# Performance work log

Hardware: AMD Instinct MI355X
Metric: run time of the kernel (lower is better)

## Reference

```python
import jax, jax.numpy as jnp
import numpy as np

BLOCK = 100  # hard-coded block size in the original module


def setup_inputs() -> dict:
    key = jax.random.key(0)
    k1, k2 = jax.random.split(key)
    N_freqs = 128
    n = N_freqs * BLOCK  # 12800
    # DPP kernel: symmetric PD so every 100x100 diagonal block has positive logdet
    R = jax.random.normal(k1, (n, n), dtype=jnp.float32) * 0.05
    L_kernel = (R + R.T) * 0.5 + 2.0 * jnp.eye(n, dtype=jnp.float32)
    weights = jax.random.normal(k2, (n,), dtype=jnp.float32)
    return {"weights": weights, "L_kernel": L_kernel, "N_freqs": N_freqs}


def reference(weights, L_kernel, N_freqs):
    # Gather the N_freqs diagonal 100x100 blocks without touching off-diagonals
    blocks4 = L_kernel.reshape(N_freqs, BLOCK, N_freqs, BLOCK)
    idx = jnp.arange(N_freqs)
    diag_blocks = blocks4[idx, :, idx, :]  # [N_freqs, 100, 100]
    s = jax.nn.sigmoid(weights).reshape(N_freqs, BLOCK)  # [N_freqs, 100]
    I = jnp.eye(BLOCK, dtype=L_kernel.dtype)
    # diag(s_i) @ (B_i - I) + I, batched over blocks
    M = s[:, :, None] * (diag_blocks - I) + I  # [N_freqs, 100, 100]
    sign, logabs = jnp.linalg.slogdet(M)
    # torch.logdet returns nan for non-positive determinant
    logdets = jnp.where(sign > 0, logabs, jnp.nan)
    within_freq_dets = jnp.sum(logdets)
    within_freq_dets_tensor = logdets.astype(jnp.float32)
    return (within_freq_dets, within_freq_dets_tensor)
```

## Files before the change

### kernel.cpp

```cpp
#include <hip/hip_runtime.h>
#include <math.h>

#define BLK 100
#define NF  128
#define NTOT (NF * BLK)
#define P   104
#define NT  512

__device__ __forceinline__ float4 fnma4(float4 v, float s, const float4 p) {
    v.x -= s * p.x; v.y -= s * p.y; v.z -= s * p.z; v.w -= s * p.w; return v;
}
__device__ __forceinline__ float4 mul4(float4 v, float s) {
    v.x *= s; v.y *= s; v.z *= s; v.w *= s; return v;
}

#define LD4(r, c4) (*reinterpret_cast<float4*>(&a[(r) * P + 4 * (c4)]))

#define PANEL_Q(kb, gq)                                                        \
    {                                                                          \
        float4 pp0 = LD4((kb) + 0, (gq));                                      \
        float4 pp1 = LD4((kb) + 1, (gq));                                      \
        float4 pp2 = LD4((kb) + 2, (gq));                                      \
        float4 pp3 = LD4((kb) + 3, (gq));                                      \
        float4 P0  = LD4((kb) + 0, gg);                                        \
        float4 P1  = LD4((kb) + 1, gg);                                        \
        float4 P2  = LD4((kb) + 2, gg);                                        \
        float4 P3  = LD4((kb) + 3, gg);                                        \
        const float d0 = pp0.x, r0i = 1.0f / d0;                               \
        float l;                                                               \
        l = pp1.x * r0i;  pp1 = fnma4(pp1, l, pp0);  P1 = fnma4(P1, l, P0);    \
        const float d1 = pp1.y, r1i = 1.0f / d1;                               \
        l = pp2.x * r0i;  pp2 = fnma4(pp2, l, pp0);  P2 = fnma4(P2, l, P0);    \
        l = pp2.y * r1i;  pp2 = fnma4(pp2, l, pp1);  P2 = fnma4(P2, l, P1);    \
        const float d2 = pp2.z, r2i = 1.0f / d2;                               \
        l = pp3.x * r0i;  pp3 = fnma4(pp3, l, pp0);  P3 = fnma4(P3, l, P0);    \
        l = pp3.y * r1i;  pp3 = fnma4(pp3, l, pp1);  P3 = fnma4(P3, l, P1);    \
        l = pp3.z * r2i;  pp3 = fnma4(pp3, l, pp2);  P3 = fnma4(P3, l, P2);    \
        const float d3 = pp3.w, r3i = 1.0f / d3;                               \
        Q3 = mul4(P3, r3i);                                                    \
        Q2 = mul4(fnma4(P2, pp2.w, Q3), r2i);                                  \
        Q1 = mul4(fnma4(fnma4(P1, pp1.z, Q2), pp1.w, Q3), r1i);                \
        Q0 = mul4(fnma4(fnma4(fnma4(P0, pp0.y, Q1), pp0.z, Q2), pp0.w, Q3), r0i); \
        mant *= d0 * d1 * d2 * d3;                                             \
        { int t_; mant = frexpf(mant, &t_); e2 += t_; }                        \
        lneg += (d0 < 0.0f) + (d1 < 0.0f) + (d2 < 0.0f) + (d3 < 0.0f);         \
    }

__global__ __launch_bounds__(NT) void lu_logdet_kernel(const float* __restrict__ w,
                                                       const float* __restrict__ L,
                                                       float* __restrict__ out) {
    __shared__ float  a[BLK * P];
    __shared__ float4 qbuf[2][4][26];

    const int f    = blockIdx.x;
    const int tid  = threadIdx.x;
    const int wave = tid >> 6;
    const int sid  = tid >> 5;
    const int g    = tid & 31;
    const int gg   = (g < 25) ? g : 24;

    const float* base = L + (size_t)f * BLK * NTOT + (size_t)f * BLK;
    for (int q = tid; q < BLK * 25; q += NT) {
        const int r  = q / 25;
        const int c0 = (q - r * 25) * 4;
        const float4 v = *reinterpret_cast<const float4*>(base + (size_t)r * NTOT + c0);
        const float sv = 1.0f / (1.0f + expf(-w[f * BLK + r]));
        const float ds = 1.0f - sv;
        float4 m;
        m.x = sv * v.x + ((c0 + 0) == r ? ds : 0.0f);
        m.y = sv * v.y + ((c0 + 1) == r ? ds : 0.0f);
        m.z = sv * v.z + ((c0 + 2) == r ? ds : 0.0f);
        m.w = sv * v.w + ((c0 + 3) == r ? ds : 0.0f);
        *reinterpret_cast<float4*>(&a[r * P + c0]) = m;
    }
    __syncthreads();

    float mant = 1.0f;
    int   e2   = 0;
    int   lneg = 0;
    float4 Q0, Q1, Q2, Q3;

    PANEL_Q(0, 0)

    for (int k0 = 0; k0 <= 92; k0 += 4) {
        const int gp = k0 >> 2;
        const int b  = gp & 1;
        const int nb = b ^ 1;

        if (wave == 0) {
            __builtin_amdgcn_s_setprio(1);
            if (g > gp && g < 25) {
                const int s  = sid & 1;
                const int i1 = k0 + 4 + s;
                const int i2 = k0 + 6 + s;
                const float4 pan1 = LD4(i1, gp);
                const float4 pan2 = LD4(i2, gp);
                float4 v1 = LD4(i1, g);
                float4 v2 = LD4(i2, g);
                v1 = fnma4(v1, pan1.x, Q0); v1 = fnma4(v1, pan1.y, Q1);
                v1 = fnma4(v1, pan1.z, Q2); v1 = fnma4(v1, pan1.w, Q3);
                v2 = fnma4(v2, pan2.x, Q0); v2 = fnma4(v2, pan2.y, Q1);
                v2 = fnma4(v2, pan2.z, Q2); v2 = fnma4(v2, pan2.w, Q3);
                LD4(i1, g) = v1;
                LD4(i2, g) = v2;
            }
            PANEL_Q(k0 + 4, gp + 1)
            if (g < 25) {
                qbuf[nb][0][g] = Q0; qbuf[nb][1][g] = Q1;
                qbuf[nb][2][g] = Q2; qbuf[nb][3][g] = Q3;
            }
            __builtin_amdgcn_s_setprio(0);
        } else {
            if (k0 > 0) {
                Q0 = qbuf[b][0][gg]; Q1 = qbuf[b][1][gg];
                Q2 = qbuf[b][2][gg]; Q3 = qbuf[b][3][gg];
            }
            if (g > gp && g < 25) {
                int i = k0 + 8 + (sid - 2);
                for (; i + 14 < BLK; i += 28) {
                    const int i2 = i + 14;
                    const float4 panA = LD4(i,  gp);
                    const float4 panB = LD4(i2, gp);
                    float4 vA = LD4(i,  g);
                    float4 vB = LD4(i2, g);
                    vA = fnma4(vA, panA.x, Q0); vA = fnma4(vA, panA.y, Q1);
                    vA = fnma4(vA, panA.z, Q2); vA = fnma4(vA, panA.w, Q3);
                    vB = fnma4(vB, panB.x, Q0); vB = fnma4(vB, panB.y, Q1);
                    vB = fnma4(vB, panB.z, Q2); vB = fnma4(vB, panB.w, Q3);
                    LD4(i,  g) = vA;
                    LD4(i2, g) = vB;
                }
                for (; i < BLK; i += 14) {
                    const float4 pan = LD4(i, gp);
                    float4 v = LD4(i, g);
                    v = fnma4(v, pan.x, Q0); v = fnma4(v, pan.y, Q1);
                    v = fnma4(v, pan.z, Q2); v = fnma4(v, pan.w, Q3);
                    LD4(i, g) = v;
                }
            }
        }
        __syncthreads();
    }

    if (tid == 0) {
        float ld = logf(mant) + (float)e2 * 0.69314718055994531f;
        if ((lneg & 1) || !isfinite(ld)) ld = __int_as_float(0x7fc00000);
        out[1 + f] = ld;
        atomicAdd(out, ld);
    }
}

extern "C" void kernel_launch(void* const* d_in, const int* in_sizes, int n_in,
                              void* d_out, int out_size, void* d_ws, size_t ws_size,
                              hipStream_t stream) {
    const float* w = (const float*)d_in[0];
    const float* L = (const float*)d_in[1];
    float* out = (float*)d_out;
    hipMemsetAsync(d_out, 0, sizeof(float), stream);
    lu_logdet_kernel<<<NF, NT, 0, stream>>>(w, L, out);
}
```

Measured before the change: 30.43 us.

## Widen blocked LU panel from 4 to 8 columns to halve barrier steps

```diff
diff --git a/kernel.cpp b/kernel.cpp
--- a/kernel.cpp
+++ b/kernel.cpp
@@ -16,41 +16,75 @@
 
 #define LD4(r, c4) (*reinterpret_cast<float4*>(&a[(r) * P + 4 * (c4)]))
 
-#define PANEL_Q(kb, gq)                                                        \
-    {                                                                          \
-        float4 pp0 = LD4((kb) + 0, (gq));                                      \
-        float4 pp1 = LD4((kb) + 1, (gq));                                      \
-        float4 pp2 = LD4((kb) + 2, (gq));                                      \
-        float4 pp3 = LD4((kb) + 3, (gq));                                      \
-        float4 P0  = LD4((kb) + 0, gg);                                        \
-        float4 P1  = LD4((kb) + 1, gg);                                        \
-        float4 P2  = LD4((kb) + 2, gg);                                        \
-        float4 P3  = LD4((kb) + 3, gg);                                        \
-        const float d0 = pp0.x, r0i = 1.0f / d0;                               \
-        float l;                                                               \
-        l = pp1.x * r0i;  pp1 = fnma4(pp1, l, pp0);  P1 = fnma4(P1, l, P0);    \
-        const float d1 = pp1.y, r1i = 1.0f / d1;                               \
-        l = pp2.x * r0i;  pp2 = fnma4(pp2, l, pp0);  P2 = fnma4(P2, l, P0);    \
-        l = pp2.y * r1i;  pp2 = fnma4(pp2, l, pp1);  P2 = fnma4(P2, l, P1);    \
-        const float d2 = pp2.z, r2i = 1.0f / d2;                               \
-        l = pp3.x * r0i;  pp3 = fnma4(pp3, l, pp0);  P3 = fnma4(P3, l, P0);    \
-        l = pp3.y * r1i;  pp3 = fnma4(pp3, l, pp1);  P3 = fnma4(P3, l, P1);    \
-        l = pp3.z * r2i;  pp3 = fnma4(pp3, l, pp2);  P3 = fnma4(P3, l, P2);    \
-        const float d3 = pp3.w, r3i = 1.0f / d3;                               \
-        Q3 = mul4(P3, r3i);                                                    \
-        Q2 = mul4(fnma4(P2, pp2.w, Q3), r2i);                                  \
-        Q1 = mul4(fnma4(fnma4(P1, pp1.z, Q2), pp1.w, Q3), r1i);                \
-        Q0 = mul4(fnma4(fnma4(fnma4(P0, pp0.y, Q1), pp0.z, Q2), pp0.w, Q3), r0i); \
-        mant *= d0 * d1 * d2 * d3;                                             \
-        { int t_; mant = frexpf(mant, &t_); e2 += t_; }                        \
-        lneg += (d0 < 0.0f) + (d1 < 0.0f) + (d2 < 0.0f) + (d3 < 0.0f);         \
-    }
-
-__global__ __launch_bounds__(NT) void lu_logdet_kernel(const float* __restrict__ w,
-                                                       const float* __restrict__ L,
-                                                       float* __restrict__ out) {
+#define PANEL_Q8(kb, q2)                                                        \
+    {                                                                           \
+        float4 pA0 = LD4((kb)+0, (q2)), pB0 = LD4((kb)+0, (q2)+1);              \
+        float4 pA1 = LD4((kb)+1, (q2)), pB1 = LD4((kb)+1, (q2)+1);              \
+        float4 pA2 = LD4((kb)+2, (q2)), pB2 = LD4((kb)+2, (q2)+1);              \
+        float4 pA3 = LD4((kb)+3, (q2)), pB3 = LD4((kb)+3, (q2)+1);              \
+        float4 pA4 = LD4((kb)+4, (q2)), pB4 = LD4((kb)+4, (q2)+1);              \
+        float4 pA5 = LD4((kb)+5, (q2)), pB5 = LD4((kb)+5, (q2)+1);              \
+        float4 pA6 = LD4((kb)+6, (q2)), pB6 = LD4((kb)+6, (q2)+1);              \
+        float4 pA7 = LD4((kb)+7, (q2)), pB7 = LD4((kb)+7, (q2)+1);              \
+        float4 P0 = LD4((kb)+0, gg), P1 = LD4((kb)+1, gg);                      \
+        float4 P2 = LD4((kb)+2, gg), P3 = LD4((kb)+3, gg);                      \
+        float4 P4 = LD4((kb)+4, gg), P5 = LD4((kb)+5, gg);                      \
+        float4 P6 = LD4((kb)+6, gg), P7 = LD4((kb)+7, gg);                      \
+        const float d0 = pA0.x, r0 = 1.0f / d0;                                 \
+        float l;                                                                \
+        l = pA1.x*r0; pA1=fnma4(pA1,l,pA0); pB1=fnma4(pB1,l,pB0); P1=fnma4(P1,l,P0); \
+        l = pA2.x*r0; pA2=fnma4(pA2,l,pA0); pB2=fnma4(pB2,l,pB0); P2=fnma4(P2,l,P0); \
+        l = pA3.x*r0; pA3=fnma4(pA3,l,pA0); pB3=fnma4(pB3,l,pB0); P3=fnma4(P3,l,P0); \
+        l = pA4.x*r0; pA4=fnma4(pA4,l,pA0); pB4=fnma4(pB4,l,pB0); P4=fnma4(P4,l,P0); \
+        l = pA5.x*r0; pA5=fnma4(pA5,l,pA0); pB5=fnma4(pB5,l,pB0); P5=fnma4(P5,l,P0); \
+        l = pA6.x*r0; pA6=fnma4(pA6,l,pA0); pB6=fnma4(pB6,l,pB0); P6=fnma4(P6,l,P0); \
+        l = pA7.x*r0; pA7=fnma4(pA7,l,pA0); pB7=fnma4(pB7,l,pB0); P7=fnma4(P7,l,P0); \
+        const float d1 = pA1.y, r1 = 1.0f / d1;                                 \
+        l = pA2.y*r1; pA2=fnma4(pA2,l,pA1); pB2=fnma4(pB2,l,pB1); P2=fnma4(P2,l,P1); \
+        l = pA3.y*r1; pA3=fnma4(pA3,l,pA1); pB3=fnma4(pB3,l,pB1); P3=fnma4(P3,l,P1); \
+        l = pA4.y*r1; pA4=fnma4(pA4,l,pA1); pB4=fnma4(pB4,l,pB1); P4=fnma4(P4,l,P1); \
+        l = pA5.y*r1; pA5=fnma4(pA5,l,pA1); pB5=fnma4(pB5,l,pB1); P5=fnma4(P5,l,P1); \
+        l = pA6.y*r1; pA6=fnma4(pA6,l,pA1); pB6=fnma4(pB6,l,pB1); P6=fnma4(P6,l,P1); \
+        l = pA7.y*r1; pA7=fnma4(pA7,l,pA1); pB7=fnma4(pB7,l,pB1); P7=fnma4(P7,l,P1); \
+        const float d2 = pA2.z, r2 = 1.0f / d2;                                 \
+        l = pA3.z*r2; pA3=fnma4(pA3,l,pA2); pB3=fnma4(pB3,l,pB2); P3=fnma4(P3,l,P2); \
+        l = pA4.z*r2; pA4=fnma4(pA4,l,pA2); pB4=fnma4(pB4,l,pB2); P4=fnma4(P4,l,P2); \
+        l = pA5.z*r2; pA5=fnma4(pA5,l,pA2); pB5=fnma4(pB5,l,pB2); P5=fnma4(P5,l,P2); \
+        l = pA6.z*r2; pA6=fnma4(pA6,l,pA2); pB6=fnma4(pB6,l,pB2); P6=fnma4(P6,l,P2); \
+        l = pA7.z*r2; pA7=fnma4(pA7,l,pA2); pB7=fnma4(pB7,l,pB2); P7=fnma4(P7,l,P2); \
+        const float d3 = pA3.w, r3 = 1.0f / d3;                                 \
+        l = pA4.w*r3; pB4=fnma4(pB4,l,pB3); P4=fnma4(P4,l,P3);                  \
+        l = pA5.w*r3; pB5=fnma4(pB5,l,pB3); P5=fnma4(P5,l,P3);                  \
+        l = pA6.w*r3; pB6=fnma4(pB6,l,pB3); P6=fnma4(P6,l,P3);                  \
+        l = pA7.w*r3; pB7=fnma4(pB7,l,pB3); P7=fnma4(P7,l,P3);                  \
+        const float d4 = pB4.x, r4 = 1.0f / d4;                                 \
+        l = pB5.x*r4; pB5=fnma4(pB5,l,pB4); P5=fnma4(P5,l,P4);                  \
+        l = pB6.x*r4; pB6=fnma4(pB6,l,pB4); P6=fnma4(P6,l,P4);                  \
+        l = pB7.x*r4; pB7=fnma4(pB7,l,pB4); P7=fnma4(P7,l,P4);                  \
+        const float d5 = pB5.y, r5 = 1.0f / d5;                                 \
+        l = pB6.y*r5; pB6=fnma4(pB6,l,pB5); P6=fnma4(P6,l,P5);                  \
+        l = pB7.y*r5; pB7=fnma4(pB7,l,pB5); P7=fnma4(P7,l,P5);                  \
+        const float d6 = pB6.z, r6 = 1.0f / d6;                                 \
+        l = pB7.z*r6; pB7=fnma4(pB7,l,pB6); P7=fnma4(P7,l,P6);                  \
+        const float d7 = pB7.w, r7 = 1.0f / d7;                                 \
+        Q7 = mul4(P7, r7);                                                      \
+        Q6 = mul4(fnma4(P6, pB6.w, Q7), r6);                                    \
+        Q5 = mul4(fnma4(fnma4(P5, pB5.z, Q6), pB5.w, Q7), r5);                  \
+        Q4 = mul4(fnma4(fnma4(fnma4(P4, pB4.y, Q5), pB4.z, Q6), pB4.w, Q7), r4); \
+        Q3 = mul4(fnma4(fnma4(fnma4(fnma4(P3, pB3.x, Q4), pB3.y, Q5), pB3.z, Q6), pB3.w, Q7), r3); \
+        Q2 = mul4(fnma4(fnma4(fnma4(fnma4(fnma4(P2, pA2.w, Q3), pB2.x, Q4), pB2.y, Q5), pB2.z, Q6), pB2.w, Q7), r2); \
+        Q1 = mul4(fnma4(fnma4(fnma4(fnma4(fnma4(fnma4(P1, pA1.z, Q2), pA1.w, Q3), pB1.x, Q4), pB1.y, Q5), pB1.z, Q6), pB1.w, Q7), r1); \
+        Q0 = mul4(fnma4(fnma4(fnma4(fnma4(fnma4(fnma4(fnma4(P0, pA0.y, Q1), pA0.z, Q2), pA0.w, Q3), pB0.x, Q4), pB0.y, Q5), pB0.z, Q6), pB0.w, Q7), r0); \
+        mant *= d0 * d1 * d2 * d3; { int t_; mant = frexpf(mant, &t_); e2 += t_; } \
+        mant *= d4 * d5 * d6 * d7; { int t_; mant = frexpf(mant, &t_); e2 += t_; } \
+        lneg += (d0<0.0f)+(d1<0.0f)+(d2<0.0f)+(d3<0.0f)+(d4<0.0f)+(d5<0.0f)+(d6<0.0f)+(d7<0.0f); \
+    }
+
+__global__ __launch_bounds__(NT, 2) void lu_logdet_kernel(const float* __restrict__ w,
+                                                          const float* __restrict__ L,
+                                                          float* __restrict__ out) {
     __shared__ float  a[BLK * P];
-    __shared__ float4 qbuf[2][4][26];
+    __shared__ float4 qbuf[2][8][26];
 
     const int f    = blockIdx.x;
     const int tid  = threadIdx.x;
@@ -78,63 +112,96 @@
     float mant = 1.0f;
     int   e2   = 0;
     int   lneg = 0;
-    float4 Q0, Q1, Q2, Q3;
-
-    PANEL_Q(0, 0)
-
-    for (int k0 = 0; k0 <= 92; k0 += 4) {
-        const int gp = k0 >> 2;
-        const int b  = gp & 1;
+    float4 Q0, Q1, Q2, Q3, Q4, Q5, Q6, Q7;
+
+    PANEL_Q8(0, 0)
+
+    for (int k0 = 0; k0 <= 88; k0 += 8) {
+        const int pc = k0 >> 2;
+        const int b  = (k0 >> 3) & 1;
         const int nb = b ^ 1;
 
         if (wave == 0) {
             __builtin_amdgcn_s_setprio(1);
-            if (g > gp && g < 25) {
-                const int s  = sid & 1;
-                const int i1 = k0 + 4 + s;
-                const int i2 = k0 + 6 + s;
-                const float4 pan1 = LD4(i1, gp);
-                const float4 pan2 = LD4(i2, gp);
-                float4 v1 = LD4(i1, g);
-                float4 v2 = LD4(i2, g);
-                v1 = fnma4(v1, pan1.x, Q0); v1 = fnma4(v1, pan1.y, Q1);
-                v1 = fnma4(v1, pan1.z, Q2); v1 = fnma4(v1, pan1.w, Q3);
-                v2 = fnma4(v2, pan2.x, Q0); v2 = fnma4(v2, pan2.y, Q1);
-                v2 = fnma4(v2, pan2.z, Q2); v2 = fnma4(v2, pan2.w, Q3);
-                LD4(i1, g) = v1;
-                LD4(i2, g) = v2;
-            }
-            PANEL_Q(k0 + 4, gp + 1)
             if (g < 25) {
-                qbuf[nb][0][g] = Q0; qbuf[nb][1][g] = Q1;
-                qbuf[nb][2][g] = Q2; qbuf[nb][3][g] = Q3;
+                const int rbase = k0 + 8 + ((sid & 1) << 2);
+                #pragma unroll
+                for (int j = 0; j < 4; ++j) {
+                    const int r = rbase + j;
+                    if (r < BLK) {
+                        const float4 pA = LD4(r, pc);
+                        const float4 pB = LD4(r, pc + 1);
+                        float4 v = LD4(r, g);
+                        v = fnma4(v, pA.x, Q0); v = fnma4(v, pA.y, Q1);
+                        v = fnma4(v, pA.z, Q2); v = fnma4(v, pA.w, Q3);
+                        v = fnma4(v, pB.x, Q4); v = fnma4(v, pB.y, Q5);
+                        v = fnma4(v, pB.z, Q6); v = fnma4(v, pB.w, Q7);
+                        LD4(r, g) = v;
+                    }
+                }
+            }
+            if (k0 < 88) {
+                PANEL_Q8(k0 + 8, pc + 2)
+                if (g < 25) {
+                    qbuf[nb][0][g] = Q0; qbuf[nb][1][g] = Q1;
+                    qbuf[nb][2][g] = Q2; qbuf[nb][3][g] = Q3;
+                    qbuf[nb][4][g] = Q4; qbuf[nb][5][g] = Q5;
+                    qbuf[nb][6][g] = Q6; qbuf[nb][7][g] = Q7;
+                }
+            } else {
+                float4 t0 = LD4(96, 24), t1 = LD4(97, 24), t2 = LD4(98, 24), t3 = LD4(99, 24);
+                const float d0 = t0.x, r0 = 1.0f / d0;
+                float l;
+                l = t1.x*r0; t1 = fnma4(t1, l, t0);
+                l = t2.x*r0; t2 = fnma4(t2, l, t0);
+                l = t3.x*r0; t3 = fnma4(t3, l, t0);
+                const float d1 = t1.y, r1 = 1.0f / d1;
+                l = t2.y*r1; t2 = fnma4(t2, l, t1);
+                l = t3.y*r1; t3 = fnma4(t3, l, t1);
+                const float d2 = t2.z, r2 = 1.0f / d2;
+                l = t3.z*r2; t3 = fnma4(t3, l, t2);
+                const float d3 = t3.w;
+                mant *= d0 * d1 * d2 * d3;
+                { int t_; mant = frexpf(mant, &t_); e2 += t_; }
+                lneg += (d0<0.0f)+(d1<0.0f)+(d2<0.0f)+(d3<0.0f);
             }
             __builtin_amdgcn_s_setprio(0);
         } else {
             if (k0 > 0) {
                 Q0 = qbuf[b][0][gg]; Q1 = qbuf[b][1][gg];
                 Q2 = qbuf[b][2][gg]; Q3 = qbuf[b][3][gg];
-            }
-            if (g > gp && g < 25) {
-                int i = k0 + 8 + (sid - 2);
+                Q4 = qbuf[b][4][gg]; Q5 = qbuf[b][5][gg];
+                Q6 = qbuf[b][6][gg]; Q7 = qbuf[b][7][gg];
+            }
+            if (g < 25) {
+                int i = k0 + 16 + (sid - 2);
                 for (; i + 14 < BLK; i += 28) {
                     const int i2 = i + 14;
-                    const float4 panA = LD4(i,  gp);
-                    const float4 panB = LD4(i2, gp);
+                    const float4 pA1_ = LD4(i,  pc);
+                    const float4 pB1_ = LD4(i,  pc + 1);
+                    const float4 pA2_ = LD4(i2, pc);
+                    const float4 pB2_ = LD4(i2, pc + 1);
                     float4 vA = LD4(i,  g);
                     float4 vB = LD4(i2, g);
-                    vA = fnma4(vA, panA.x, Q0); vA = fnma4(vA, panA.y, Q1);
-                    vA = fnma4(vA, panA.z, Q2); vA = fnma4(vA, panA.w, Q3);
-                    vB = fnma4(vB, panB.x, Q0); vB = fnma4(vB, panB.y, Q1);
-                    vB = fnma4(vB, panB.z, Q2); vB = fnma4(vB, panB.w, Q3);
+                    vA = fnma4(vA, pA1_.x, Q0); vA = fnma4(vA, pA1_.y, Q1);
+                    vA = fnma4(vA, pA1_.z, Q2); vA = fnma4(vA, pA1_.w, Q3);
+                    vA = fnma4(vA, pB1_.x, Q4); vA = fnma4(vA, pB1_.y, Q5);
+                    vA = fnma4(vA, pB1_.z, Q6); vA = fnma4(vA, pB1_.w, Q7);
+                    vB = fnma4(vB, pA2_.x, Q0); vB = fnma4(vB, pA2_.y, Q1);
+                    vB = fnma4(vB, pA2_.z, Q2); vB = fnma4(vB, pA2_.w, Q3);
+                    vB = fnma4(vB, pB2_.x, Q4); vB = fnma4(vB, pB2_.y, Q5);
+                    vB = fnma4(vB, pB2_.z, Q6); vB = fnma4(vB, pB2_.w, Q7);
                     LD4(i,  g) = vA;
                     LD4(i2, g) = vB;
                 }
                 for (; i < BLK; i += 14) {
-                    const float4 pan = LD4(i, gp);
+                    const float4 pA = LD4(i, pc);
+                    const float4 pB = LD4(i, pc + 1);
                     float4 v = LD4(i, g);
-                    v = fnma4(v, pan.x, Q0); v = fnma4(v, pan.y, Q1);
-                    v = fnma4(v, pan.z, Q2); v = fnma4(v, pan.w, Q3);
+                    v = fnma4(v, pA.x, Q0); v = fnma4(v, pA.y, Q1);
+                    v = fnma4(v, pA.z, Q2); v = fnma4(v, pA.w, Q3);
+                    v = fnma4(v, pB.x, Q4); v = fnma4(v, pB.y, Q5);
+                    v = fnma4(v, pB.z, Q6); v = fnma4(v, pB.w, Q7);
                     LD4(i, g) = v;
                 }
             }
```

After: 33.63 us. 1.11x slower.

## Build next LU panel in registers via lane shuffles, unroll trailing update

Applied to the files above, without the earlier changes.

```diff
diff --git a/kernel.cpp b/kernel.cpp
--- a/kernel.cpp
+++ b/kernel.cpp
@@ -13,19 +13,20 @@
 __device__ __forceinline__ float4 mul4(float4 v, float s) {
     v.x *= s; v.y *= s; v.z *= s; v.w *= s; return v;
 }
+__device__ __forceinline__ float rdl(float x, int l) {
+    return __uint_as_float(__builtin_amdgcn_readlane(__float_as_uint(x), l));
+}
+__device__ __forceinline__ float4 swap32(float4 v) {
+    float4 o;
+    o.x = __shfl_xor(v.x, 32); o.y = __shfl_xor(v.y, 32);
+    o.z = __shfl_xor(v.z, 32); o.w = __shfl_xor(v.w, 32);
+    return o;
+}
 
 #define LD4(r, c4) (*reinterpret_cast<float4*>(&a[(r) * P + 4 * (c4)]))
 
-#define PANEL_Q(kb, gq)                                                        \
+#define PANEL_CORE()                                                           \
     {                                                                          \
-        float4 pp0 = LD4((kb) + 0, (gq));                                      \
-        float4 pp1 = LD4((kb) + 1, (gq));                                      \
-        float4 pp2 = LD4((kb) + 2, (gq));                                      \
-        float4 pp3 = LD4((kb) + 3, (gq));                                      \
-        float4 P0  = LD4((kb) + 0, gg);                                        \
-        float4 P1  = LD4((kb) + 1, gg);                                        \
-        float4 P2  = LD4((kb) + 2, gg);                                        \
-        float4 P3  = LD4((kb) + 3, gg);                                        \
         const float d0 = pp0.x, r0i = 1.0f / d0;                               \
         float l;                                                               \
         l = pp1.x * r0i;  pp1 = fnma4(pp1, l, pp0);  P1 = fnma4(P1, l, P0);    \
@@ -46,6 +47,10 @@
         lneg += (d0 < 0.0f) + (d1 < 0.0f) + (d2 < 0.0f) + (d3 < 0.0f);         \
     }
 
+#define SWEEP4(vv, pan)                                                        \
+    vv = fnma4(vv, pan.x, Q0); vv = fnma4(vv, pan.y, Q1);                      \
+    vv = fnma4(vv, pan.z, Q2); vv = fnma4(vv, pan.w, Q3);
+
 __global__ __launch_bounds__(NT) void lu_logdet_kernel(const float* __restrict__ w,
                                                        const float* __restrict__ L,
                                                        float* __restrict__ out) {
@@ -58,6 +63,7 @@
     const int sid  = tid >> 5;
     const int g    = tid & 31;
     const int gg   = (g < 25) ? g : 24;
+    const int h    = sid & 1;
 
     const float* base = L + (size_t)f * BLK * NTOT + (size_t)f * BLK;
     for (int q = tid; q < BLK * 25; q += NT) {
@@ -80,7 +86,11 @@
     int   lneg = 0;
     float4 Q0, Q1, Q2, Q3;
 
-    PANEL_Q(0, 0)
+    {
+        float4 pp0 = LD4(0, 0), pp1 = LD4(1, 0), pp2 = LD4(2, 0), pp3 = LD4(3, 0);
+        float4 P0 = LD4(0, gg), P1 = LD4(1, gg), P2 = LD4(2, gg), P3 = LD4(3, gg);
+        PANEL_CORE()
+    }
 
     for (int k0 = 0; k0 <= 92; k0 += 4) {
         const int gp = k0 >> 2;
@@ -89,22 +99,26 @@
 
         if (wave == 0) {
             __builtin_amdgcn_s_setprio(1);
-            if (g > gp && g < 25) {
-                const int s  = sid & 1;
-                const int i1 = k0 + 4 + s;
-                const int i2 = k0 + 6 + s;
-                const float4 pan1 = LD4(i1, gp);
-                const float4 pan2 = LD4(i2, gp);
-                float4 v1 = LD4(i1, g);
-                float4 v2 = LD4(i2, g);
-                v1 = fnma4(v1, pan1.x, Q0); v1 = fnma4(v1, pan1.y, Q1);
-                v1 = fnma4(v1, pan1.z, Q2); v1 = fnma4(v1, pan1.w, Q3);
-                v2 = fnma4(v2, pan2.x, Q0); v2 = fnma4(v2, pan2.y, Q1);
-                v2 = fnma4(v2, pan2.z, Q2); v2 = fnma4(v2, pan2.w, Q3);
-                LD4(i1, g) = v1;
-                LD4(i2, g) = v2;
-            }
-            PANEL_Q(k0 + 4, gp + 1)
+            const int i1 = k0 + 4 + h;
+            const int i2 = k0 + 6 + h;
+            const float4 pan1 = LD4(i1, gp);
+            const float4 pan2 = LD4(i2, gp);
+            float4 v1 = LD4(i1, gg);
+            float4 v2 = LD4(i2, gg);
+            SWEEP4(v1, pan1)
+            SWEEP4(v2, pan2)
+            const float4 o1 = swap32(v1);
+            const float4 o2 = swap32(v2);
+            float4 P0 = h ? o1 : v1;
+            float4 P1 = h ? v1 : o1;
+            float4 P2 = h ? o2 : v2;
+            float4 P3 = h ? v2 : o2;
+            const int gq = gp + 1;
+            float4 pp0 = make_float4(rdl(P0.x, gq), rdl(P0.y, gq), rdl(P0.z, gq), rdl(P0.w, gq));
+            float4 pp1 = make_float4(rdl(P1.x, gq), rdl(P1.y, gq), rdl(P1.z, gq), rdl(P1.w, gq));
+            float4 pp2 = make_float4(rdl(P2.x, gq), rdl(P2.y, gq), rdl(P2.z, gq), rdl(P2.w, gq));
+            float4 pp3 = make_float4(rdl(P3.x, gq), rdl(P3.y, gq), rdl(P3.z, gq), rdl(P3.w, gq));
+            PANEL_CORE()
             if (g < 25) {
                 qbuf[nb][0][g] = Q0; qbuf[nb][1][g] = Q1;
                 qbuf[nb][2][g] = Q2; qbuf[nb][3][g] = Q3;
@@ -117,25 +131,35 @@
             }
             if (g > gp && g < 25) {
                 int i = k0 + 8 + (sid - 2);
+                for (; i + 42 < BLK; i += 56) {
+                    const float4 pa = LD4(i,      gp);
+                    const float4 pb = LD4(i + 14, gp);
+                    const float4 pc = LD4(i + 28, gp);
+                    const float4 pd = LD4(i + 42, gp);
+                    float4 va = LD4(i,      g);
+                    float4 vb = LD4(i + 14, g);
+                    float4 vc = LD4(i + 28, g);
+                    float4 vd = LD4(i + 42, g);
+                    SWEEP4(va, pa) SWEEP4(vb, pb) SWEEP4(vc, pc) SWEEP4(vd, pd)
+                    LD4(i,      g) = va;
+                    LD4(i + 14, g) = vb;
+                    LD4(i + 28, g) = vc;
+                    LD4(i + 42, g) = vd;
+                }
                 for (; i + 14 < BLK; i += 28) {
-                    const int i2 = i + 14;
-                    const float4 panA = LD4(i,  gp);
-                    const float4 panB = LD4(i2, gp);
-                    float4 vA = LD4(i,  g);
-                    float4 vB = LD4(i2, g);
-                    vA = fnma4(vA, panA.x, Q0); vA = fnma4(vA, panA.y, Q1);
-                    vA = fnma4(vA, panA.z, Q2); vA = fnma4(vA, panA.w, Q3);
-                    vB = fnma4(vB, panB.x, Q0); vB = fnma4(vB, panB.y, Q1);
-                    vB = fnma4(vB, panB.z, Q2); vB = fnma4(vB, panB.w, Q3);
-                    LD4(i,  g) = vA;
-                    LD4(i2, g) = vB;
+                    const float4 pa = LD4(i,      gp);
+                    const float4 pb = LD4(i + 14, gp);
+                    float4 va = LD4(i,      g);
+                    float4 vb = LD4(i + 14, g);
+                    SWEEP4(va, pa) SWEEP4(vb, pb)
+                    LD4(i,      g) = va;
+                    LD4(i + 14, g) = vb;
                 }
                 for (; i < BLK; i += 14) {
-                    const float4 pan = LD4(i, gp);
-                    float4 v = LD4(i, g);
-                    v = fnma4(v, pan.x, Q0); v = fnma4(v, pan.y, Q1);
-                    v = fnma4(v, pan.z, Q2); v = fnma4(v, pan.w, Q3);
-                    LD4(i, g) = v;
+                    const float4 pa = LD4(i, gp);
+                    float4 va = LD4(i, g);
+                    SWEEP4(va, pa)
+                    LD4(i, g) = va;
                 }
             }
         }
```

Result: slower. 31.79 us (+4.5%).

## Process two 4-column panels per barrier phase in blocked LU logdet

Applied to the files above, without the earlier changes.

```diff
diff --git a/kernel.cpp b/kernel.cpp
--- a/kernel.cpp
+++ b/kernel.cpp
@@ -46,11 +46,15 @@
         lneg += (d0 < 0.0f) + (d1 < 0.0f) + (d2 < 0.0f) + (d3 < 0.0f);         \
     }
 
+#define SWEEPQ(vv, pan, Qa, Qb, Qc, Qd)                                        \
+    vv = fnma4(vv, pan.x, Qa); vv = fnma4(vv, pan.y, Qb);                      \
+    vv = fnma4(vv, pan.z, Qc); vv = fnma4(vv, pan.w, Qd);
+
 __global__ __launch_bounds__(NT) void lu_logdet_kernel(const float* __restrict__ w,
                                                        const float* __restrict__ L,
                                                        float* __restrict__ out) {
     __shared__ float  a[BLK * P];
-    __shared__ float4 qbuf[2][4][26];
+    __shared__ float4 qbuf[2][2][4][26];
 
     const int f    = blockIdx.x;
     const int tid  = threadIdx.x;
@@ -58,6 +62,7 @@
     const int sid  = tid >> 5;
     const int g    = tid & 31;
     const int gg   = (g < 25) ? g : 24;
+    const int h    = sid & 1;
 
     const float* base = L + (size_t)f * BLK * NTOT + (size_t)f * BLK;
     for (int q = tid; q < BLK * 25; q += NT) {
@@ -81,60 +86,121 @@
     float4 Q0, Q1, Q2, Q3;
 
     PANEL_Q(0, 0)
-
-    for (int k0 = 0; k0 <= 92; k0 += 4) {
+    float4 QA0 = Q0, QA1 = Q1, QA2 = Q2, QA3 = Q3;
+    float4 QB0, QB1, QB2, QB3;
+    if (wave == 0) {
+        const int r0 = 4 + h, r1 = 6 + h;
+        float4 p0 = LD4(r0, 0), p1 = LD4(r1, 0);
+        float4 v0 = LD4(r0, gg), v1 = LD4(r1, gg);
+        SWEEPQ(v0, p0, QA0, QA1, QA2, QA3)
+        SWEEPQ(v1, p1, QA0, QA1, QA2, QA3)
+        if (g < 25) { LD4(r0, g) = v0; LD4(r1, g) = v1; }
+        PANEL_Q(4, 1)
+        QB0 = Q0; QB1 = Q1; QB2 = Q2; QB3 = Q3;
+        if (g < 25) {
+            qbuf[0][1][0][g] = QB0; qbuf[0][1][1][g] = QB1;
+            qbuf[0][1][2][g] = QB2; qbuf[0][1][3][g] = QB3;
+        }
+    }
+    __syncthreads();
+
+    for (int k0 = 0; k0 <= 88; k0 += 8) {
         const int gp = k0 >> 2;
-        const int b  = gp & 1;
+        const int ph = k0 >> 3;
+        const int b  = ph & 1;
         const int nb = b ^ 1;
 
         if (wave == 0) {
             __builtin_amdgcn_s_setprio(1);
-            if (g > gp && g < 25) {
-                const int s  = sid & 1;
-                const int i1 = k0 + 4 + s;
-                const int i2 = k0 + 6 + s;
-                const float4 pan1 = LD4(i1, gp);
-                const float4 pan2 = LD4(i2, gp);
-                float4 v1 = LD4(i1, g);
-                float4 v2 = LD4(i2, g);
-                v1 = fnma4(v1, pan1.x, Q0); v1 = fnma4(v1, pan1.y, Q1);
-                v1 = fnma4(v1, pan1.z, Q2); v1 = fnma4(v1, pan1.w, Q3);
-                v2 = fnma4(v2, pan2.x, Q0); v2 = fnma4(v2, pan2.y, Q1);
-                v2 = fnma4(v2, pan2.z, Q2); v2 = fnma4(v2, pan2.w, Q3);
-                LD4(i1, g) = v1;
-                LD4(i2, g) = v2;
-            }
-            PANEL_Q(k0 + 4, gp + 1)
-            if (g < 25) {
-                qbuf[nb][0][g] = Q0; qbuf[nb][1][g] = Q1;
-                qbuf[nb][2][g] = Q2; qbuf[nb][3][g] = Q3;
+            const int r0 = k0 + 8 + h,  r1 = k0 + 10 + h;
+            const int r2 = k0 + 12 + h, r3 = k0 + 14 + h;
+            const bool t23 = (r2 < BLK);
+            float4 v0, v1, v2, v3;
+            {
+                const float4 p0 = LD4(r0, gp), p1 = LD4(r1, gp);
+                v0 = LD4(r0, gg); v1 = LD4(r1, gg);
+                SWEEPQ(v0, p0, QA0, QA1, QA2, QA3)
+                SWEEPQ(v1, p1, QA0, QA1, QA2, QA3)
+                if (g < 25) { LD4(r0, g) = v0; LD4(r1, g) = v1; }
+                if (t23) {
+                    const float4 p2 = LD4(r2, gp), p3 = LD4(r3, gp);
+                    v2 = LD4(r2, gg); v3 = LD4(r3, gg);
+                    SWEEPQ(v2, p2, QA0, QA1, QA2, QA3)
+                    SWEEPQ(v3, p3, QA0, QA1, QA2, QA3)
+                    if (g < 25) { LD4(r2, g) = v2; LD4(r3, g) = v3; }
+                }
+            }
+            {
+                const float4 p0 = LD4(r0, gp + 1), p1 = LD4(r1, gp + 1);
+                SWEEPQ(v0, p0, QB0, QB1, QB2, QB3)
+                SWEEPQ(v1, p1, QB0, QB1, QB2, QB3)
+                if (g < 25) { LD4(r0, g) = v0; LD4(r1, g) = v1; }
+                if (t23) {
+                    const float4 p2 = LD4(r2, gp + 1), p3 = LD4(r3, gp + 1);
+                    SWEEPQ(v2, p2, QB0, QB1, QB2, QB3)
+                    SWEEPQ(v3, p3, QB0, QB1, QB2, QB3)
+                    if (g < 25) { LD4(r2, g) = v2; LD4(r3, g) = v3; }
+                }
+            }
+            if (k0 < 88) {
+                PANEL_Q(k0 + 8, gp + 2)
+                QA0 = Q0; QA1 = Q1; QA2 = Q2; QA3 = Q3;
+                if (g < 25) {
+                    qbuf[nb][0][0][g] = QA0; qbuf[nb][0][1][g] = QA1;
+                    qbuf[nb][0][2][g] = QA2; qbuf[nb][0][3][g] = QA3;
+                }
+                {
+                    const float4 p2 = LD4(r2, gp + 2), p3 = LD4(r3, gp + 2);
+                    SWEEPQ(v2, p2, QA0, QA1, QA2, QA3)
+                    SWEEPQ(v3, p3, QA0, QA1, QA2, QA3)
+                    if (g < 25) { LD4(r2, g) = v2; LD4(r3, g) = v3; }
+                }
+                PANEL_Q(k0 + 12, gp + 3)
+                QB0 = Q0; QB1 = Q1; QB2 = Q2; QB3 = Q3;
+                if (g < 25) {
+                    qbuf[nb][1][0][g] = QB0; qbuf[nb][1][1][g] = QB1;
+                    qbuf[nb][1][2][g] = QB2; qbuf[nb][1][3][g] = QB3;
+                }
+            } else {
+                PANEL_Q(96, 24)
             }
             __builtin_amdgcn_s_setprio(0);
         } else {
+            float4 CA0, CA1, CA2, CA3, CB0, CB1, CB2, CB3;
             if (k0 > 0) {
-                Q0 = qbuf[b][0][gg]; Q1 = qbuf[b][1][gg];
-                Q2 = qbuf[b][2][gg]; Q3 = qbuf[b][3][gg];
-            }
+                CA0 = qbuf[b][0][0][gg]; CA1 = qbuf[b][0][1][gg];
+                CA2 = qbuf[b][0][2][gg]; CA3 = qbuf[b][0][3][gg];
+            } else {
+                CA0 = QA0; CA1 = QA1; CA2 = QA2; CA3 = QA3;
+            }
+            CB0 = qbuf[b][1][0][gg]; CB1 = qbuf[b][1][1][gg];
+            CB2 = qbuf[b][1][2][gg]; CB3 = qbuf[b][1][3][gg];
             if (g > gp && g < 25) {
-                int i = k0 + 8 + (sid - 2);
+                int i = k0 + 16 + (sid - 2);
                 for (; i + 14 < BLK; i += 28) {
                     const int i2 = i + 14;
-                    const float4 panA = LD4(i,  gp);
-                    const float4 panB = LD4(i2, gp);
-                    float4 vA = LD4(i,  g);
-                    float4 vB = LD4(i2, g);
-                    vA = fnma4(vA, panA.x, Q0); vA = fnma4(vA, panA.y, Q1);
-                    vA = fnma4(vA, panA.z, Q2); vA = fnma4(vA, panA.w, Q3);
-                    vB = fnma4(vB, panB.x, Q0); vB = fnma4(vB, panB.y, Q1);
-                    vB = fnma4(vB, panB.z, Q2); vB = fnma4(vB, panB.w, Q3);
-                    LD4(i,  g) = vA;
-                    LD4(i2, g) = vB;
+                    const float4 pa1 = LD4(i,  gp);
+                    const float4 pa2 = LD4(i2, gp);
+                    float4 va = LD4(i,  g);
+                    float4 vb = LD4(i2, g);
+                    SWEEPQ(va, pa1, CA0, CA1, CA2, CA3)
+                    SWEEPQ(vb, pa2, CA0, CA1, CA2, CA3)
+                    LD4(i,  g) = va;
+                    LD4(i2, g) = vb;
+                    const float4 pb1 = LD4(i,  gp + 1);
+                    const float4 pb2 = LD4(i2, gp + 1);
+                    SWEEPQ(va, pb1, CB0, CB1, CB2, CB3)
+                    SWEEPQ(vb, pb2, CB0, CB1, CB2, CB3)
+                    LD4(i,  g) = va;
+                    LD4(i2, g) = vb;
                 }
                 for (; i < BLK; i += 14) {
-                    const float4 pan = LD4(i, gp);
+                    const float4 pa = LD4(i, gp);
                     float4 v = LD4(i, g);
-                    v = fnma4(v, pan.x, Q0); v = fnma4(v, pan.y, Q1);
-                    v = fnma4(v, pan.z, Q2); v = fnma4(v, pan.w, Q3);
+                    SWEEPQ(v, pa, CA0, CA1, CA2, CA3)
+                    LD4(i, g) = v;
+                    const float4 pb = LD4(i, gp + 1);
+                    SWEEPQ(v, pb, CB0, CB1, CB2, CB3)
                     LD4(i, g) = v;
                 }
             }
```

Measured after the change: 33.44 us. +9.9%, slower.
